# Optimization experiments

Measured on AMD Instinct MI355X. Metric: run time of the kernel, lower is better.

The kernel has to match this reference:

```python
import jax, jax.numpy as jnp
import numpy as np

B, T, DU, DM, DA, DF = 8, 2048, 512, 512, 256, 12
L_STAGES = 4   # number of routing stages
R_ITERS = 1    # diversity refinement iterations in selector
GAMMA = 1.0    # coverage_gamma
EPS = 1e-6
SCALE = float(np.sqrt(DA))


def setup_inputs() -> dict:
    key = jax.random.key(0)
    ks = jax.random.split(key, 16)
    w = lambda k, shape, fan_in: (jax.random.normal(k, shape, jnp.float32) / np.sqrt(fan_in)).astype(jnp.float32)
    return {
        'u': jax.random.normal(ks[0], (B, T, DU), jnp.float32),
        'structural_features': jax.random.normal(ks[1], (B, T, DF), jnp.float32),
        'similarity': jax.random.uniform(ks[2], (B, T, T), jnp.float32),
        'memory0': jax.random.normal(ks[3], (B, DM), jnp.float32),
        'Wq': w(ks[4], (DA, DM), DM),
        'Wk': w(ks[5], (DA, DU), DU),
        'Wv': w(ks[6], (DU, DU), DU),
        'sb_w1': w(ks[7], (DA, 3), 3),
        'sb_b1': jnp.zeros((DA,), jnp.float32),
        'sb_w2': w(ks[8], (1, DA), DA),
        'sb_b2': jnp.zeros((1,), jnp.float32),
        'log_temp': jnp.zeros((), jnp.float32),
        'W_ih': w(ks[9], (3 * DM, DU + 4), DU + 4),
        'b_ih': jnp.zeros((3 * DM,), jnp.float32),
        'W_hh': w(ks[10], (3 * DM, DM), DM),
        'b_hh': jnp.zeros((3 * DM,), jnp.float32),
    }


def _selection_stats(y, u):
    # y: [B,T], u: [B,T,DU] -> c: [B,4]
    Tn = u.shape[1]
    y_sum = jnp.maximum(y.sum(axis=1), EPS)                      # [B]
    coverage = y.sum(axis=1) / Tn
    y_norm = y / y_sum[:, None]
    entropy = -(y_norm * jnp.log(jnp.maximum(y_norm, EPS))).sum(axis=1)
    centroid = jnp.einsum('bt,btd->bd', y, u)                    # unnormalized [B,DU]
    cen = centroid / y_sum[:, None]
    dist = jnp.linalg.norm(u - cen[:, None, :], axis=-1)         # [B,T]
    spread = (y * dist).sum(axis=1) / y_sum
    wsq = (y * jnp.sum(u * u, axis=-1)).sum(axis=1)              # [B]
    csq = jnp.sum(centroid * centroid, axis=1)
    compact = 2.0 * (y_sum * wsq - csq) / jnp.maximum(y_sum * y_sum, EPS)
    return jnp.stack([coverage, entropy, spread, compact], axis=1)


def reference(u, structural_features, similarity, memory0, Wq, Wk, Wv,
              sb_w1, sb_b1, sb_w2, sb_b2, log_temp, W_ih, b_ih, W_hh, b_hh):
    k = jnp.einsum('btu,au->bta', u, Wk)                         # [B,T,DA]
    v = jnp.einsum('btu,vu->btv', u, Wv)                         # [B,T,DU]
    desc = structural_features[..., -4:-1]                       # [B,T,3]
    sbias = (jax.nn.gelu(desc @ sb_w1.T + sb_b1, approximate=False) @ sb_w2.T + sb_b2)[..., 0]
    temp = jnp.clip(jnp.exp(log_temp), 0.1, 10.0)
    memory = memory0
    prev = None
    outs = []
    for _ in range(L_STAGES):
        q = memory @ Wq.T                                        # [B,DA]
        scores = jnp.einsum('bta,ba->bt', k, q) / SCALE + sbias
        if prev is not None:
            scores = scores - GAMMA * jnp.einsum('bts,bs->bt', similarity, prev)
        logits = scores / temp
        y = jax.nn.softmax(logits, axis=1)
        for _r in range(R_ITERS):
            overlap = jnp.einsum('bts,bs->bt', similarity, y)
            penalty = overlap / jnp.maximum(jnp.max(overlap, axis=1, keepdims=True), EPS)
            logits = logits - penalty
            y = jax.nn.softmax(logits, axis=1)
        z = jnp.einsum('bt,btd->bd', y, v)                       # stage token [B,DU]
        c = _selection_stats(y, u)                               # [B,4]
        x = jnp.concatenate([z, c], axis=-1)
        gi = x @ W_ih.T + b_ih
        gh = memory @ W_hh.T + b_hh
        gir, giz, gin = jnp.split(gi, 3, axis=-1)
        ghr, ghz, ghn = jnp.split(gh, 3, axis=-1)
        rg = jax.nn.sigmoid(gir + ghr)
        zg = jax.nn.sigmoid(giz + ghz)
        ng = jnp.tanh(gin + rg * ghn)
        memory = (1.0 - zg) * ng + zg * memory                   # GRUCell update
        prev = y if prev is None else prev + y
        outs.append(z)
    return jnp.stack(outs, axis=1)                               # [B,L,DU]
```

## Files before the change

kernel.cpp:

```cpp
#include <hip/hip_runtime.h>
#include <math.h>

constexpr int cB = 8, cT = 2048, cDU = 512, cDM = 512, cDA = 256, cDF = 12, cL = 4;
constexpr float cEPS = 1e-6f;
constexpr float cSCALE = 16.0f;
constexpr float cGAMMA = 1.0f;

typedef unsigned short u16;
typedef unsigned char u8;
typedef u16 u16x8 __attribute__((ext_vector_type(8)));

constexpr size_t F_SB = 0;
constexpr size_t F_UN = F_SB + 16384;
constexpr size_t F_LG = F_UN + 16384;
constexpr size_t F_Y  = F_LG + 16384;
constexpr size_t F_PR = F_Y  + 16384;
constexpr size_t F_OV = F_PR + 16384;
constexpr size_t F_SP = F_OV + 16384;
constexpr size_t F_QK = F_SP + 256;
constexpr size_t F_M0 = F_QK + 4096;
constexpr size_t F_M1 = F_M0 + 4096;
constexpr size_t F_C  = F_M1 + 4096;
constexpr size_t F_Z  = F_C  + 4096;
constexpr size_t F_SC = F_Z  + 4096;
constexpr size_t F_A  = F_SC + 64;
constexpr size_t F_END = F_A + 262144;
constexpr size_t U_OFFB   = F_END * 4;
constexpr size_t U_BYTES  = (size_t)cB * cT * cDU * 2;
constexpr size_t S8_OFFB  = U_OFFB + U_BYTES;
constexpr size_t S8_BYTES = (size_t)cB * cT * cT;
constexpr size_t WS_NEED_U   = S8_OFFB;
constexpr size_t WS_NEED_ALL = S8_OFFB + S8_BYTES;

__device__ __forceinline__ float wave_sum(float v) {
#pragma unroll
  for (int o = 32; o; o >>= 1) v += __shfl_down(v, o);
  return v;
}
__device__ __forceinline__ u16 f2bf(float f) {
  unsigned u = __float_as_uint(f);
  return (u16)((u + 0x7fffu + ((u >> 16) & 1u)) >> 16);
}
__device__ __forceinline__ float bf2f(u16 h) { return __uint_as_float(((unsigned)h) << 16); }
__device__ __forceinline__ float dot4(float4 a, float4 b) {
  return a.x * b.x + a.y * b.y + a.z * b.z + a.w * b.w;
}
__device__ __forceinline__ unsigned pack4(float a, float b, float c, float d) {
  unsigned b0 = (unsigned)(a * 255.f + 0.5f);
  unsigned b1 = (unsigned)(b * 255.f + 0.5f);
  unsigned b2 = (unsigned)(c * 255.f + 0.5f);
  unsigned b3 = (unsigned)(d * 255.f + 0.5f);
  return b0 | (b1 << 8) | (b2 << 16) | (b3 << 24);
}
__device__ __forceinline__ void dotu8(float& sd, unsigned w, float4 p) {
  sd += (float)(w & 255u) * p.x + (float)((w >> 8) & 255u) * p.y +
        (float)((w >> 16) & 255u) * p.z + (float)(w >> 24) * p.w;
}

__global__ __launch_bounds__(256) void k_init(
    const float* __restrict__ u, const float* __restrict__ sf,
    const float* __restrict__ mem0,
    const float* __restrict__ Wq, const float* __restrict__ Wk,
    const float* __restrict__ w1, const float* __restrict__ b1,
    const float* __restrict__ w2, const float* __restrict__ b2,
    float* __restrict__ wsf, u16* __restrict__ ubf, int use_ubf) {
  const int tid = threadIdx.x;
  if (blockIdx.x >= 1024) {
    __shared__ float wkj[32][8];
    int j0 = (blockIdx.x - 1024) * 8;
    float acc[8][2] = {};
    for (int a0 = 0; a0 < cDA; a0 += 32) {
      wkj[tid >> 3][tid & 7] = Wk[(size_t)(a0 + (tid >> 3)) * cDU + j0 + (tid & 7)];
      __syncthreads();
#pragma unroll 8
      for (int aa = 0; aa < 32; ++aa) {
        float wq0 = Wq[(size_t)(a0 + aa) * cDM + tid * 2];
        float wq1 = Wq[(size_t)(a0 + aa) * cDM + tid * 2 + 1];
#pragma unroll
        for (int r = 0; r < 8; ++r) {
          acc[r][0] += wkj[aa][r] * wq0;
          acc[r][1] += wkj[aa][r] * wq1;
        }
      }
      __syncthreads();
    }
#pragma unroll
    for (int r = 0; r < 8; ++r) {
      wsf[F_A + (size_t)(j0 + r) * cDU + tid * 2] = acc[r][0];
      wsf[F_A + (size_t)(j0 + r) * cDU + tid * 2 + 1] = acc[r][1];
    }
    return;
  }
  const int gt = blockIdx.x * 256 + tid;
  const int nt = 1024 * 256;
  const int wv = tid >> 6, lane = tid & 63;
  const int gw = blockIdx.x * 4 + wv;
  const int nw = 1024 * 4;

  for (int i = gt; i < cB * cDM; i += nt) wsf[F_M0 + i] = mem0[i];

  if (use_ubf) {
    const int NU8 = cB * cT * cDU / 8;
    const float4* src = (const float4*)u;
    for (int c = gt; c < NU8; c += nt) {
      float4 f0 = src[(size_t)c * 2], f1 = src[(size_t)c * 2 + 1];
      u16x8 o;
      o[0] = f2bf(f0.x); o[1] = f2bf(f0.y); o[2] = f2bf(f0.z); o[3] = f2bf(f0.w);
      o[4] = f2bf(f1.x); o[5] = f2bf(f1.y); o[6] = f2bf(f1.z); o[7] = f2bf(f1.w);
      *(u16x8*)(ubf + (size_t)c * 8) = o;
    }
  }
  for (int row = gw; row < cB * cT; row += nw) {
    float d0 = sf[(size_t)row * cDF + 8];
    float d1 = sf[(size_t)row * cDF + 9];
    float d2 = sf[(size_t)row * cDF + 10];
    float acc = 0.f;
#pragma unroll
    for (int i = 0; i < 4; ++i) {
      int a = lane * 4 + i;
      float h = d0 * w1[a * 3 + 0] + d1 * w1[a * 3 + 1] + d2 * w1[a * 3 + 2] + b1[a];
      float g = 0.5f * h * (1.0f + erff(h * 0.70710678118654752f));
      acc += g * w2[a];
    }
    float un = 0.f;
    const float4* ur = (const float4*)(u + (size_t)row * cDU);
#pragma unroll
    for (int m = 0; m < 2; ++m) { float4 x = ur[lane + m * 64]; un += dot4(x, x); }
    acc = wave_sum(acc);
    un = wave_sum(un);
    if (lane == 0) { wsf[F_SB + row] = acc + b2[0]; wsf[F_UN + row] = un; }
  }
}

__global__ __launch_bounds__(256) void k_qk(const float* __restrict__ A,
                                            const float* __restrict__ mem,
                                            float* __restrict__ qk,
                                            float* __restrict__ c_raw) {
  int wv = threadIdx.x >> 6, lane = threadIdx.x & 63;
  int wid = blockIdx.x * 4 + wv;
  int b = wid >> 9, j = wid & 511;
  const float4* ar = (const float4*)(A + (size_t)j * cDM);
  const float4* mr = (const float4*)(mem + (size_t)b * cDM);
  float acc = dot4(ar[lane * 2], mr[lane * 2]) + dot4(ar[lane * 2 + 1], mr[lane * 2 + 1]);
  acc = wave_sum(acc);
  if (lane == 0) qk[b * cDU + j] = acc;
  int gt = blockIdx.x * 256 + threadIdx.x;
  if (gt < cB * cDU) c_raw[gt] = 0.f;
}

__global__ __launch_bounds__(256) void k_scores(
    const u16* __restrict__ ubf, const float* __restrict__ uf,
    const float* __restrict__ qk, const float* __restrict__ sbias,
    const u8* __restrict__ sim8, const float* __restrict__ simf,
    const float* __restrict__ prev, const float* __restrict__ log_temp,
    float gamma, int use_ubf, int use_s8, float* __restrict__ logits) {
  int wid = (blockIdx.x * blockDim.x + threadIdx.x) >> 6;
  int lane = threadIdx.x & 63;
  int b = wid >> 11;
  const float4* qk4 = (const float4*)(qk + (size_t)b * cDU);
  float4 q0 = qk4[lane * 2], q1 = qk4[lane * 2 + 1];
  float acc;
  if (use_ubf) {
    u16x8 s = *(const u16x8*)(ubf + (size_t)wid * cDU + lane * 8);
    acc = bf2f(s[0]) * q0.x + bf2f(s[1]) * q0.y + bf2f(s[2]) * q0.z + bf2f(s[3]) * q0.w +
          bf2f(s[4]) * q1.x + bf2f(s[5]) * q1.y + bf2f(s[6]) * q1.z + bf2f(s[7]) * q1.w;
  } else {
    const float4* ur = (const float4*)(uf + (size_t)wid * cDU);
    acc = dot4(ur[lane * 2], q0) + dot4(ur[lane * 2 + 1], q1);
  }
  acc *= (1.0f / cSCALE);
  if (gamma != 0.0f) {
    float sd = 0.f;
    const float4* pr4 = (const float4*)(prev + (size_t)b * cT);
    if (use_s8) {
#pragma unroll
      for (int m = 0; m < 2; ++m) {
        uint4 sq = *(const uint4*)(sim8 + (size_t)wid * cT + m * 1024 + lane * 16);
        const float4* pb = pr4 + m * 256 + lane * 4;
        dotu8(sd, sq.x, pb[0]); dotu8(sd, sq.y, pb[1]);
        dotu8(sd, sq.z, pb[2]); dotu8(sd, sq.w, pb[3]);
      }
      sd *= (1.0f / 255.0f);
    } else {
      const float4* sr = (const float4*)(simf + (size_t)wid * cT);
#pragma unroll
      for (int m = 0; m < 8; ++m) sd += dot4(sr[lane + m * 64], pr4[lane + m * 64]);
    }
    acc -= gamma * sd;
  }
  acc = wave_sum(acc);
  if (lane == 0) {
    float temp = fminf(fmaxf(expf(log_temp[0]), 0.1f), 10.0f);
    logits[wid] = (acc + sbias[wid]) / temp;
  }
}

__global__ __launch_bounds__(256) void k_overlap(
    const u8* __restrict__ sim8c, u8* __restrict__ sim8w,
    const float* __restrict__ simf,
    const float* __restrict__ logits, int use_s8, int convert,
    float* __restrict__ overlap) {
  __shared__ float ylds[2176];
  __shared__ float red[256];
  const int tid = threadIdx.x;
  const int wv = tid >> 6, lane = tid & 63;
  const int b = blockIdx.x >> 7;
  float l[8];
  float mx = -INFINITY;
#pragma unroll
  for (int e = 0; e < 8; ++e) { l[e] = logits[b * cT + e * 256 + tid]; mx = fmaxf(mx, l[e]); }
  red[tid] = mx; __syncthreads();
  for (int s2 = 128; s2; s2 >>= 1) { if (tid < s2) red[tid] = fmaxf(red[tid], red[tid + s2]); __syncthreads(); }
  mx = red[0]; __syncthreads();
  float sum = 0.f;
#pragma unroll
  for (int e = 0; e < 8; ++e) {
    float ev = expf(l[e] - mx);
    sum += ev;
    int s = e * 256 + tid;
    ylds[s + (s >> 4)] = ev;
  }
  red[tid] = sum; __syncthreads();
  for (int s2 = 128; s2; s2 >>= 1) { if (tid < s2) red[tid] += red[tid + s2]; __syncthreads(); }
  float invS = 1.f / red[0];
  __syncthreads();
  for (int r = 0; r < 4; ++r) {
    int row = blockIdx.x * 16 + wv * 4 + r;
    float acc = 0.f;
    if (use_s8 && !convert) {
#pragma unroll
      for (int m = 0; m < 2; ++m) {
        uint4 sq = *(const uint4*)(sim8c + (size_t)row * cT + m * 1024 + lane * 16);
        int s0 = m * 1024 + lane * 16;
#pragma unroll
        for (int k = 0; k < 4; ++k) {
          unsigned w = (&sq.x)[k];
          int s = s0 + k * 4;
          acc += (float)(w & 255u)         * ylds[s + (s >> 4)] +
                 (float)((w >> 8) & 255u)  * ylds[(s + 1) + ((s + 1) >> 4)] +
                 (float)((w >> 16) & 255u) * ylds[(s + 2) + ((s + 2) >> 4)] +
                 (float)(w >> 24)          * ylds[(s + 3) + ((s + 3) >> 4)];
        }
      }
      acc *= (1.0f / 255.0f);
    } else {
#pragma unroll
      for (int m = 0; m < 2; ++m) {
        const float4* sr = (const float4*)(simf + (size_t)row * cT + m * 1024 + lane * 16);
        uint4 oq;
#pragma unroll
        for (int k = 0; k < 4; ++k) {
          float4 sv = sr[k];
          int s = m * 1024 + lane * 16 + k * 4;
          acc += sv.x * ylds[s + (s >> 4)] + sv.y * ylds[(s + 1) + ((s + 1) >> 4)] +
                 sv.z * ylds[(s + 2) + ((s + 2) >> 4)] + sv.w * ylds[(s + 3) + ((s + 3) >> 4)];
          (&oq.x)[k] = pack4(sv.x, sv.y, sv.z, sv.w);
        }
        if (convert)
          *(uint4*)(sim8w + (size_t)row * cT + m * 1024 + lane * 16) = oq;
      }
    }
    acc = wave_sum(acc);
    if (lane == 0) overlap[row] = acc * invS;
  }
}

__global__ __launch_bounds__(256) void k_statcen(
    const float* __restrict__ overlap, const float* __restrict__ logits,
    const float* __restrict__ unorm2,
    const u16* __restrict__ ubf, const float* __restrict__ uf, int use_ubf,
    float* __restrict__ y, float* __restrict__ prev,
    float* __restrict__ scal, float* __restrict__ c_raw, int first_stage) {
  __shared__ float ylds[2048];
  __shared__ float comb[2048];
  __shared__ float red[256];
  const int tid = threadIdx.x;
  const int wv = tid >> 6, lane = tid & 63;
  const int ch = blockIdx.x, b = blockIdx.y;
  float o[8], l[8], yv[8];
  float mo = -INFINITY;
#pragma unroll
  for (int e = 0; e < 8; ++e) { o[e] = overlap[b * cT + e * 256 + tid]; mo = fmaxf(mo, o[e]); }
  red[tid] = mo; __syncthreads();
  for (int s2 = 128; s2; s2 >>= 1) { if (tid < s2) red[tid] = fmaxf(red[tid], red[tid + s2]); __syncthreads(); }
  mo = fmaxf(red[0], cEPS); __syncthreads();
  float ml = -INFINITY;
#pragma unroll
  for (int e = 0; e < 8; ++e) { l[e] = logits[b * cT + e * 256 + tid] - o[e] / mo; ml = fmaxf(ml, l[e]); }
  red[tid] = ml; __syncthreads();
  for (int s2 = 128; s2; s2 >>= 1) { if (tid < s2) red[tid] = fmaxf(red[tid], red[tid + s2]); __syncthreads(); }
  ml = red[0]; __syncthreads();
  float sum = 0.f;
#pragma unroll
  for (int e = 0; e < 8; ++e) { l[e] = expf(l[e] - ml); sum += l[e]; }
  red[tid] = sum; __syncthreads();
  for (int s2 = 128; s2; s2 >>= 1) { if (tid < s2) red[tid] += red[tid + s2]; __syncthreads(); }
  float inv = 1.f / red[0]; __syncthreads();
  float ysr_p = 0.f, wsq_p = 0.f;
#pragma unroll
  for (int e = 0; e < 8; ++e) {
    yv[e] = l[e] * inv;
    ylds[e * 256 + tid] = yv[e];
    ysr_p += yv[e];
    wsq_p += yv[e] * unorm2[b * cT + e * 256 + tid];
  }
  red[tid] = ysr_p; __syncthreads();
  for (int s2 = 128; s2; s2 >>= 1) { if (tid < s2) red[tid] += red[tid + s2]; __syncthreads(); }
  float ysr = red[0]; __syncthreads();
  float ysc = fmaxf(ysr, cEPS);
  red[tid] = wsq_p; __syncthreads();
  for (int s2 = 128; s2; s2 >>= 1) { if (tid < s2) red[tid] += red[tid + s2]; __syncthreads(); }
  float wsq = red[0]; __syncthreads();
  float ent_p = 0.f;
#pragma unroll
  for (int e = 0; e < 8; ++e) {
    float yn = yv[e] / ysc;
    ent_p -= yn * logf(fmaxf(yn, cEPS));
  }
  red[tid] = ent_p; __syncthreads();
  for (int s2 = 128; s2; s2 >>= 1) { if (tid < s2) red[tid] += red[tid + s2]; __syncthreads(); }
  float ent = red[0]; __syncthreads();
  if (ch == 0) {
#pragma unroll
    for (int e = 0; e < 8; ++e) {
      int idx = b * cT + e * 256 + tid;
      y[idx] = yv[e];
      if (first_stage) prev[idx] = yv[e]; else prev[idx] += yv[e];
    }
    if (tid == 0) {
      scal[b * 8 + 0] = ysc;
      scal[b * 8 + 1] = ysr / (float)cT;
      scal[b * 8 + 2] = ent;
      scal[b * 8 + 3] = wsq;
    }
  }
  float acc[8] = {};
  for (int i = 0; i < 16; ++i) {
    int r = ch * 64 + wv * 16 + i;
    float yvv = ylds[r];
    int row = b * cT + r;
    if (use_ubf) {
      u16x8 s8 = *(const u16x8*)(ubf + (size_t)row * cDU + lane * 8);
#pragma unroll
      for (int e = 0; e < 8; ++e) acc[e] += yvv * bf2f(s8[e]);
    } else {
      const float4* ur = (const float4*)(uf + (size_t)row * cDU);
      float4 a0 = ur[lane * 2], a1 = ur[lane * 2 + 1];
      acc[0] += yvv * a0.x; acc[1] += yvv * a0.y; acc[2] += yvv * a0.z; acc[3] += yvv * a0.w;
      acc[4] += yvv * a1.x; acc[5] += yvv * a1.y; acc[6] += yvv * a1.z; acc[7] += yvv * a1.w;
    }
  }
  __syncthreads();
#pragma unroll
  for (int e = 0; e < 8; ++e) comb[wv * 512 + lane * 8 + e] = acc[e];
  __syncthreads();
  float s0 = comb[tid] + comb[512 + tid] + comb[1024 + tid] + comb[1536 + tid];
  float s1 = comb[tid + 256] + comb[512 + tid + 256] + comb[1024 + tid + 256] + comb[1536 + tid + 256];
  atomicAdd(&c_raw[b * cDU + tid], s0);
  atomicAdd(&c_raw[b * cDU + tid + 256], s1);
}

__global__ __launch_bounds__(256) void k_zyd(
    const float* __restrict__ c_raw, const float* __restrict__ Wv,
    const u16* __restrict__ ubf, const float* __restrict__ uf, int use_ubf,
    const float* __restrict__ unorm2, const float* __restrict__ y,
    float* __restrict__ z, float* __restrict__ scal, float* __restrict__ sprp) {
  __shared__ float s4[4];
  int wv = threadIdx.x >> 6, lane = threadIdx.x & 63;
  if (blockIdx.x < 1024) {
    int wid = blockIdx.x * 4 + wv;
    int b = wid >> 9, j = wid & 511;
    const float4* c4 = (const float4*)(c_raw + (size_t)b * cDU);
    const float4* w4 = (const float4*)(Wv + (size_t)j * cDU);
    float acc = dot4(c4[lane * 2], w4[lane * 2]) + dot4(c4[lane * 2 + 1], w4[lane * 2 + 1]);
    acc = wave_sum(acc);
    if (lane == 0) z[b * cDU + j] = acc;
    return;
  }
  int unit = blockIdx.x - 1024;
  int b = unit >> 5, tc = unit & 31;
  float ysc = scal[b * 8 + 0];
  float inv = 1.f / ysc;
  const float4* c4 = (const float4*)(c_raw + (size_t)b * cDU);
  float4 cr0 = c4[lane * 2], cr1 = c4[lane * 2 + 1];
  float4 cx0, cx1;
  cx0.x = cr0.x * inv; cx0.y = cr0.y * inv; cx0.z = cr0.z * inv; cx0.w = cr0.w * inv;
  cx1.x = cr1.x * inv; cx1.y = cr1.y * inv; cx1.z = cr1.z * inv; cx1.w = cr1.w * inv;
  float cen2 = wave_sum(dot4(cx0, cx0) + dot4(cx1, cx1));
  if (tc == 0 && wv == 0) {
    float csq = wave_sum(dot4(cr0, cr0) + dot4(cr1, cr1));
    if (lane == 0) scal[b * 8 + 6] = csq;
  }
  float part = 0.f;
  for (int i = 0; i < 16; ++i) {
    int row = b * cT + tc * 64 + wv * 16 + i;
    float dot;
    if (use_ubf) {
      u16x8 s = *(const u16x8*)(ubf + (size_t)row * cDU + lane * 8);
      dot = bf2f(s[0]) * cx0.x + bf2f(s[1]) * cx0.y + bf2f(s[2]) * cx0.z + bf2f(s[3]) * cx0.w +
            bf2f(s[4]) * cx1.x + bf2f(s[5]) * cx1.y + bf2f(s[6]) * cx1.z + bf2f(s[7]) * cx1.w;
    } else {
      const float4* ur = (const float4*)(uf + (size_t)row * cDU);
      dot = dot4(ur[lane * 2], cx0) + dot4(ur[lane * 2 + 1], cx1);
    }
    dot = wave_sum(dot);
    if (lane == 0) {
      float d2 = unorm2[row] - 2.f * dot + cen2;
      part += y[row] * sqrtf(fmaxf(d2, 0.f));
    }
  }
  if (lane == 0) s4[wv] = part;
  __syncthreads();
  if (threadIdx.x == 0) sprp[b * 32 + tc] = s4[0] + s4[1] + s4[2] + s4[3];
}

__global__ __launch_bounds__(256) void k_gru(const float* __restrict__ z,
                                             const float* __restrict__ scal,
                                             const float* __restrict__ sprp,
                                             const float* __restrict__ memin,
                                             float* __restrict__ memout,
                                             const float* __restrict__ W_ih,
                                             const float* __restrict__ b_ih,
                                             const float* __restrict__ W_hh,
                                             const float* __restrict__ b_hh,
                                             float* __restrict__ out, int stage) {
  int wid = blockIdx.x * 4 + (threadIdx.x >> 6);
  int lane = threadIdx.x & 63;
  int b = wid >> 9, i = wid & 511;
  const float4* xz = (const float4*)(z + (size_t)b * cDU);
  const float4* xm = (const float4*)(memin + (size_t)b * cDM);
  float4 z0 = xz[lane * 2], z1 = xz[lane * 2 + 1];
  float4 m0 = xm[lane * 2], m1 = xm[lane * 2 + 1];
  float ysc = scal[b * 8 + 0];
  float sv = (lane < 32) ? sprp[b * 32 + lane] : 0.f;
  float spr_raw = wave_sum(sv);
  float aI[3], aH[3];
#pragma unroll
  for (int g = 0; g < 3; ++g) {
    size_t row = (size_t)(g * 512 + i);
    const float4* wI = (const float4*)(W_ih + row * 516);
    float a = dot4(z0, wI[lane * 2]) + dot4(z1, wI[lane * 2 + 1]);
    if (lane == 0) {
      float4 wt = wI[128];
      float cov = scal[b * 8 + 1], ent = scal[b * 8 + 2];
      float spr = spr_raw / ysc;
      float cmp = 2.f * (ysc * scal[b * 8 + 3] - scal[b * 8 + 6]) / fmaxf(ysc * ysc, cEPS);
      a += cov * wt.x + ent * wt.y + spr * wt.z + cmp * wt.w;
    }
    aI[g] = wave_sum(a);
    const float4* wH = (const float4*)(W_hh + row * cDM);
    float h = dot4(m0, wH[lane * 2]) + dot4(m1, wH[lane * 2 + 1]);
    aH[g] = wave_sum(h);
  }
  if (lane == 0) {
    float gir = aI[0] + b_ih[i],        ghr = aH[0] + b_hh[i];
    float giz = aI[1] + b_ih[512 + i],  ghz = aH[1] + b_hh[512 + i];
    float gin = aI[2] + b_ih[1024 + i], ghn = aH[2] + b_hh[1024 + i];
    float rg = 1.f / (1.f + expf(-(gir + ghr)));
    float zg = 1.f / (1.f + expf(-(giz + ghz)));
    float ng = tanhf(gin + rg * ghn);
    float mold = memin[b * cDM + i];
    memout[b * cDM + i] = (1.f - zg) * ng + zg * mold;
    out[(size_t)(b * cL + stage) * cDU + i] = z[b * cDU + i];
  }
}

extern "C" void kernel_launch(void* const* d_in, const int* in_sizes, int n_in,
                              void* d_out, int out_size, void* d_ws, size_t ws_size,
                              hipStream_t stream) {
  const float* u    = (const float*)d_in[0];
  const float* sf   = (const float*)d_in[1];
  const float* sim  = (const float*)d_in[2];
  const float* mem0 = (const float*)d_in[3];
  const float* Wq   = (const float*)d_in[4];
  const float* Wk   = (const float*)d_in[5];
  const float* Wv   = (const float*)d_in[6];
  const float* sbw1 = (const float*)d_in[7];
  const float* sbb1 = (const float*)d_in[8];
  const float* sbw2 = (const float*)d_in[9];
  const float* sbb2 = (const float*)d_in[10];
  const float* logt = (const float*)d_in[11];
  const float* W_ih = (const float*)d_in[12];
  const float* b_ih = (const float*)d_in[13];
  const float* W_hh = (const float*)d_in[14];
  const float* b_hh = (const float*)d_in[15];
  float* out = (float*)d_out;
  float* ws  = (float*)d_ws;
  u16* ubf  = (u16*)((char*)d_ws + U_OFFB);
  u8* sim8  = (u8*)((char*)d_ws + S8_OFFB);

  const int use_ubf = (ws_size >= WS_NEED_U) ? 1 : 0;
  const int use_s8  = (ws_size >= WS_NEED_ALL) ? 1 : 0;

  k_init<<<1088, 256, 0, stream>>>(u, sf, mem0, Wq, Wk, sbw1, sbb1, sbw2, sbb2,
                                   ws, ubf, use_ubf);

  for (int stage = 0; stage < cL; ++stage) {
    float* mcur = ws + ((stage & 1) ? F_M1 : F_M0);
    float* mnxt = ws + ((stage & 1) ? F_M0 : F_M1);
    k_qk<<<1024, 256, 0, stream>>>(ws + F_A, mcur, ws + F_QK, ws + F_C);
    k_scores<<<4096, 256, 0, stream>>>(ubf, u, ws + F_QK, ws + F_SB, sim8, sim,
                                       ws + F_PR, logt, stage == 0 ? 0.0f : cGAMMA,
                                       use_ubf, use_s8, ws + F_LG);
    k_overlap<<<1024, 256, 0, stream>>>(sim8, sim8, sim, ws + F_LG, use_s8,
                                        (stage == 0 && use_s8) ? 1 : 0, ws + F_OV);
    k_statcen<<<dim3(32, cB), 256, 0, stream>>>(ws + F_OV, ws + F_LG, ws + F_UN,
                                                ubf, u, use_ubf,
                                                ws + F_Y, ws + F_PR, ws + F_SC, ws + F_C,
                                                stage == 0 ? 1 : 0);
    k_zyd<<<1280, 256, 0, stream>>>(ws + F_C, Wv, ubf, u, use_ubf,
                                    ws + F_UN, ws + F_Y, ws + F_Z, ws + F_SC, ws + F_SP);
    k_gru<<<1024, 256, 0, stream>>>(ws + F_Z, ws + F_SC, ws + F_SP, mcur, mnxt,
                                    W_ih, b_ih, W_hh, b_hh, out, stage);
  }
}
```

Measured before the change: 503.4 us.

## Fuse per-stage kernels into one persistent cooperative kernel with grid syncs

Replaces the six per-stage kernel launches (qk, scores, overlap, statcen, zyd, gru) across four stages with one cooperative persistent kernel that loops over stages and phases and separates them with grid-wide barriers. The aim is to remove about 24 launch overheads and the pipeline drains between dependent small kernels. Work is redistributed over a grid sized from occupancy, capped at 1024 blocks, and the spread partials are now per-row-group (4096 entries) rather than 256. In exchange, each grid sync costs something, parallelism is capped by co-residency, and the cached static block count assumes occupancy never changes.

```diff
diff --git a/kernel.cpp b/kernel.cpp
--- a/kernel.cpp
+++ b/kernel.cpp
@@ -1,5 +1,8 @@
 #include <hip/hip_runtime.h>
+#include <hip/hip_cooperative_groups.h>
 #include <math.h>
+
+namespace cg = cooperative_groups;
 
 constexpr int cB = 8, cT = 2048, cDU = 512, cDM = 512, cDA = 256, cDF = 12, cL = 4;
 constexpr float cEPS = 1e-6f;
@@ -17,7 +20,7 @@
 constexpr size_t F_PR = F_Y  + 16384;
 constexpr size_t F_OV = F_PR + 16384;
 constexpr size_t F_SP = F_OV + 16384;
-constexpr size_t F_QK = F_SP + 256;
+constexpr size_t F_QK = F_SP + 4096;
 constexpr size_t F_M0 = F_QK + 4096;
 constexpr size_t F_M1 = F_M0 + 4096;
 constexpr size_t F_C  = F_M1 + 4096;
@@ -36,6 +39,25 @@
 #pragma unroll
   for (int o = 32; o; o >>= 1) v += __shfl_down(v, o);
   return v;
+}
+__device__ __forceinline__ float wave_max(float v) {
+#pragma unroll
+  for (int o = 32; o; o >>= 1) v = fmaxf(v, __shfl_down(v, o));
+  return v;
+}
+__device__ __forceinline__ float blk_max(float v, float* red, int wv, int lane) {
+  v = wave_max(v);
+  __syncthreads();
+  if (lane == 0) red[wv] = v;
+  __syncthreads();
+  return fmaxf(fmaxf(red[0], red[1]), fmaxf(red[2], red[3]));
+}
+__device__ __forceinline__ float blk_sum(float v, float* red, int wv, int lane) {
+  v = wave_sum(v);
+  __syncthreads();
+  if (lane == 0) red[wv] = v;
+  __syncthreads();
+  return red[0] + red[1] + red[2] + red[3];
 }
 __device__ __forceinline__ u16 f2bf(float f) {
   unsigned u = __float_as_uint(f);
@@ -95,7 +117,7 @@
   const int nt = 1024 * 256;
   const int wv = tid >> 6, lane = tid & 63;
   const int gw = blockIdx.x * 4 + wv;
-  const int nw = 1024 * 4;
+  const int nwv = 1024 * 4;
 
   for (int i = gt; i < cB * cDM; i += nt) wsf[F_M0 + i] = mem0[i];
 
@@ -110,7 +132,7 @@
       *(u16x8*)(ubf + (size_t)c * 8) = o;
     }
   }
-  for (int row = gw; row < cB * cT; row += nw) {
+  for (int row = gw; row < cB * cT; row += nwv) {
     float d0 = sf[(size_t)row * cDF + 8];
     float d1 = sf[(size_t)row * cDF + 9];
     float d2 = sf[(size_t)row * cDF + 10];
@@ -132,336 +154,324 @@
   }
 }
 
-__global__ __launch_bounds__(256) void k_qk(const float* __restrict__ A,
-                                            const float* __restrict__ mem,
-                                            float* __restrict__ qk,
-                                            float* __restrict__ c_raw) {
-  int wv = threadIdx.x >> 6, lane = threadIdx.x & 63;
-  int wid = blockIdx.x * 4 + wv;
-  int b = wid >> 9, j = wid & 511;
-  const float4* ar = (const float4*)(A + (size_t)j * cDM);
-  const float4* mr = (const float4*)(mem + (size_t)b * cDM);
-  float acc = dot4(ar[lane * 2], mr[lane * 2]) + dot4(ar[lane * 2 + 1], mr[lane * 2 + 1]);
-  acc = wave_sum(acc);
-  if (lane == 0) qk[b * cDU + j] = acc;
-  int gt = blockIdx.x * 256 + threadIdx.x;
-  if (gt < cB * cDU) c_raw[gt] = 0.f;
-}
-
-__global__ __launch_bounds__(256) void k_scores(
-    const u16* __restrict__ ubf, const float* __restrict__ uf,
-    const float* __restrict__ qk, const float* __restrict__ sbias,
-    const u8* __restrict__ sim8, const float* __restrict__ simf,
-    const float* __restrict__ prev, const float* __restrict__ log_temp,
-    float gamma, int use_ubf, int use_s8, float* __restrict__ logits) {
-  int wid = (blockIdx.x * blockDim.x + threadIdx.x) >> 6;
-  int lane = threadIdx.x & 63;
-  int b = wid >> 11;
-  const float4* qk4 = (const float4*)(qk + (size_t)b * cDU);
-  float4 q0 = qk4[lane * 2], q1 = qk4[lane * 2 + 1];
-  float acc;
-  if (use_ubf) {
-    u16x8 s = *(const u16x8*)(ubf + (size_t)wid * cDU + lane * 8);
-    acc = bf2f(s[0]) * q0.x + bf2f(s[1]) * q0.y + bf2f(s[2]) * q0.z + bf2f(s[3]) * q0.w +
-          bf2f(s[4]) * q1.x + bf2f(s[5]) * q1.y + bf2f(s[6]) * q1.z + bf2f(s[7]) * q1.w;
-  } else {
-    const float4* ur = (const float4*)(uf + (size_t)wid * cDU);
-    acc = dot4(ur[lane * 2], q0) + dot4(ur[lane * 2 + 1], q1);
-  }
-  acc *= (1.0f / cSCALE);
-  if (gamma != 0.0f) {
-    float sd = 0.f;
-    const float4* pr4 = (const float4*)(prev + (size_t)b * cT);
-    if (use_s8) {
-#pragma unroll
-      for (int m = 0; m < 2; ++m) {
-        uint4 sq = *(const uint4*)(sim8 + (size_t)wid * cT + m * 1024 + lane * 16);
-        const float4* pb = pr4 + m * 256 + lane * 4;
-        dotu8(sd, sq.x, pb[0]); dotu8(sd, sq.y, pb[1]);
-        dotu8(sd, sq.z, pb[2]); dotu8(sd, sq.w, pb[3]);
-      }
-      sd *= (1.0f / 255.0f);
-    } else {
-      const float4* sr = (const float4*)(simf + (size_t)wid * cT);
-#pragma unroll
-      for (int m = 0; m < 8; ++m) sd += dot4(sr[lane + m * 64], pr4[lane + m * 64]);
-    }
-    acc -= gamma * sd;
-  }
-  acc = wave_sum(acc);
-  if (lane == 0) {
-    float temp = fminf(fmaxf(expf(log_temp[0]), 0.1f), 10.0f);
-    logits[wid] = (acc + sbias[wid]) / temp;
-  }
-}
-
-__global__ __launch_bounds__(256) void k_overlap(
-    const u8* __restrict__ sim8c, u8* __restrict__ sim8w,
-    const float* __restrict__ simf,
-    const float* __restrict__ logits, int use_s8, int convert,
-    float* __restrict__ overlap) {
-  __shared__ float ylds[2176];
-  __shared__ float red[256];
+__global__ __launch_bounds__(256, 4) void k_main(
+    const float* __restrict__ u, const float* __restrict__ sim,
+    const float* __restrict__ logt, const float* __restrict__ Wv,
+    const float* __restrict__ W_ih, const float* __restrict__ b_ih,
+    const float* __restrict__ W_hh, const float* __restrict__ b_hh,
+    float* __restrict__ ws, u16* __restrict__ ubf, u8* __restrict__ sim8,
+    float* __restrict__ out, int use_ubf, int use_s8) {
+  cg::grid_group gg = cg::this_grid();
+  __shared__ float lds[4104];
+  float* red = lds + 4096;
   const int tid = threadIdx.x;
   const int wv = tid >> 6, lane = tid & 63;
-  const int b = blockIdx.x >> 7;
-  float l[8];
-  float mx = -INFINITY;
-#pragma unroll
-  for (int e = 0; e < 8; ++e) { l[e] = logits[b * cT + e * 256 + tid]; mx = fmaxf(mx, l[e]); }
-  red[tid] = mx; __syncthreads();
-  for (int s2 = 128; s2; s2 >>= 1) { if (tid < s2) red[tid] = fmaxf(red[tid], red[tid + s2]); __syncthreads(); }
-  mx = red[0]; __syncthreads();
-  float sum = 0.f;
-#pragma unroll
-  for (int e = 0; e < 8; ++e) {
-    float ev = expf(l[e] - mx);
-    sum += ev;
-    int s = e * 256 + tid;
-    ylds[s + (s >> 4)] = ev;
-  }
-  red[tid] = sum; __syncthreads();
-  for (int s2 = 128; s2; s2 >>= 1) { if (tid < s2) red[tid] += red[tid + s2]; __syncthreads(); }
-  float invS = 1.f / red[0];
-  __syncthreads();
-  for (int r = 0; r < 4; ++r) {
-    int row = blockIdx.x * 16 + wv * 4 + r;
-    float acc = 0.f;
-    if (use_s8 && !convert) {
-#pragma unroll
-      for (int m = 0; m < 2; ++m) {
-        uint4 sq = *(const uint4*)(sim8c + (size_t)row * cT + m * 1024 + lane * 16);
-        int s0 = m * 1024 + lane * 16;
-#pragma unroll
-        for (int k = 0; k < 4; ++k) {
-          unsigned w = (&sq.x)[k];
-          int s = s0 + k * 4;
-          acc += (float)(w & 255u)         * ylds[s + (s >> 4)] +
-                 (float)((w >> 8) & 255u)  * ylds[(s + 1) + ((s + 1) >> 4)] +
-                 (float)((w >> 16) & 255u) * ylds[(s + 2) + ((s + 2) >> 4)] +
-                 (float)(w >> 24)          * ylds[(s + 3) + ((s + 3) >> 4)];
-        }
-      }
-      acc *= (1.0f / 255.0f);
-    } else {
-#pragma unroll
-      for (int m = 0; m < 2; ++m) {
-        const float4* sr = (const float4*)(simf + (size_t)row * cT + m * 1024 + lane * 16);
-        uint4 oq;
-#pragma unroll
-        for (int k = 0; k < 4; ++k) {
-          float4 sv = sr[k];
-          int s = m * 1024 + lane * 16 + k * 4;
-          acc += sv.x * ylds[s + (s >> 4)] + sv.y * ylds[(s + 1) + ((s + 1) >> 4)] +
-                 sv.z * ylds[(s + 2) + ((s + 2) >> 4)] + sv.w * ylds[(s + 3) + ((s + 3) >> 4)];
-          (&oq.x)[k] = pack4(sv.x, sv.y, sv.z, sv.w);
-        }
-        if (convert)
-          *(uint4*)(sim8w + (size_t)row * cT + m * 1024 + lane * 16) = oq;
-      }
-    }
-    acc = wave_sum(acc);
-    if (lane == 0) overlap[row] = acc * invS;
-  }
-}
-
-__global__ __launch_bounds__(256) void k_statcen(
-    const float* __restrict__ overlap, const float* __restrict__ logits,
-    const float* __restrict__ unorm2,
-    const u16* __restrict__ ubf, const float* __restrict__ uf, int use_ubf,
-    float* __restrict__ y, float* __restrict__ prev,
-    float* __restrict__ scal, float* __restrict__ c_raw, int first_stage) {
-  __shared__ float ylds[2048];
-  __shared__ float comb[2048];
-  __shared__ float red[256];
-  const int tid = threadIdx.x;
-  const int wv = tid >> 6, lane = tid & 63;
-  const int ch = blockIdx.x, b = blockIdx.y;
-  float o[8], l[8], yv[8];
-  float mo = -INFINITY;
-#pragma unroll
-  for (int e = 0; e < 8; ++e) { o[e] = overlap[b * cT + e * 256 + tid]; mo = fmaxf(mo, o[e]); }
-  red[tid] = mo; __syncthreads();
-  for (int s2 = 128; s2; s2 >>= 1) { if (tid < s2) red[tid] = fmaxf(red[tid], red[tid + s2]); __syncthreads(); }
-  mo = fmaxf(red[0], cEPS); __syncthreads();
-  float ml = -INFINITY;
-#pragma unroll
-  for (int e = 0; e < 8; ++e) { l[e] = logits[b * cT + e * 256 + tid] - o[e] / mo; ml = fmaxf(ml, l[e]); }
-  red[tid] = ml; __syncthreads();
-  for (int s2 = 128; s2; s2 >>= 1) { if (tid < s2) red[tid] = fmaxf(red[tid], red[tid + s2]); __syncthreads(); }
-  ml = red[0]; __syncthreads();
-  float sum = 0.f;
-#pragma unroll
-  for (int e = 0; e < 8; ++e) { l[e] = expf(l[e] - ml); sum += l[e]; }
-  red[tid] = sum; __syncthreads();
-  for (int s2 = 128; s2; s2 >>= 1) { if (tid < s2) red[tid] += red[tid + s2]; __syncthreads(); }
-  float inv = 1.f / red[0]; __syncthreads();
-  float ysr_p = 0.f, wsq_p = 0.f;
-#pragma unroll
-  for (int e = 0; e < 8; ++e) {
-    yv[e] = l[e] * inv;
-    ylds[e * 256 + tid] = yv[e];
-    ysr_p += yv[e];
-    wsq_p += yv[e] * unorm2[b * cT + e * 256 + tid];
-  }
-  red[tid] = ysr_p; __syncthreads();
-  for (int s2 = 128; s2; s2 >>= 1) { if (tid < s2) red[tid] += red[tid + s2]; __syncthreads(); }
-  float ysr = red[0]; __syncthreads();
-  float ysc = fmaxf(ysr, cEPS);
-  red[tid] = wsq_p; __syncthreads();
-  for (int s2 = 128; s2; s2 >>= 1) { if (tid < s2) red[tid] += red[tid + s2]; __syncthreads(); }
-  float wsq = red[0]; __syncthreads();
-  float ent_p = 0.f;
-#pragma unroll
-  for (int e = 0; e < 8; ++e) {
-    float yn = yv[e] / ysc;
-    ent_p -= yn * logf(fmaxf(yn, cEPS));
-  }
-  red[tid] = ent_p; __syncthreads();
-  for (int s2 = 128; s2; s2 >>= 1) { if (tid < s2) red[tid] += red[tid + s2]; __syncthreads(); }
-  float ent = red[0]; __syncthreads();
-  if (ch == 0) {
-#pragma unroll
-    for (int e = 0; e < 8; ++e) {
-      int idx = b * cT + e * 256 + tid;
-      y[idx] = yv[e];
-      if (first_stage) prev[idx] = yv[e]; else prev[idx] += yv[e];
-    }
-    if (tid == 0) {
-      scal[b * 8 + 0] = ysc;
-      scal[b * 8 + 1] = ysr / (float)cT;
-      scal[b * 8 + 2] = ent;
-      scal[b * 8 + 3] = wsq;
-    }
-  }
-  float acc[8] = {};
-  for (int i = 0; i < 16; ++i) {
-    int r = ch * 64 + wv * 16 + i;
-    float yvv = ylds[r];
-    int row = b * cT + r;
-    if (use_ubf) {
-      u16x8 s8 = *(const u16x8*)(ubf + (size_t)row * cDU + lane * 8);
-#pragma unroll
-      for (int e = 0; e < 8; ++e) acc[e] += yvv * bf2f(s8[e]);
-    } else {
-      const float4* ur = (const float4*)(uf + (size_t)row * cDU);
-      float4 a0 = ur[lane * 2], a1 = ur[lane * 2 + 1];
-      acc[0] += yvv * a0.x; acc[1] += yvv * a0.y; acc[2] += yvv * a0.z; acc[3] += yvv * a0.w;
-      acc[4] += yvv * a1.x; acc[5] += yvv * a1.y; acc[6] += yvv * a1.z; acc[7] += yvv * a1.w;
-    }
-  }
-  __syncthreads();
-#pragma unroll
-  for (int e = 0; e < 8; ++e) comb[wv * 512 + lane * 8 + e] = acc[e];
-  __syncthreads();
-  float s0 = comb[tid] + comb[512 + tid] + comb[1024 + tid] + comb[1536 + tid];
-  float s1 = comb[tid + 256] + comb[512 + tid + 256] + comb[1024 + tid + 256] + comb[1536 + tid + 256];
-  atomicAdd(&c_raw[b * cDU + tid], s0);
-  atomicAdd(&c_raw[b * cDU + tid + 256], s1);
-}
-
-__global__ __launch_bounds__(256) void k_zyd(
-    const float* __restrict__ c_raw, const float* __restrict__ Wv,
-    const u16* __restrict__ ubf, const float* __restrict__ uf, int use_ubf,
-    const float* __restrict__ unorm2, const float* __restrict__ y,
-    float* __restrict__ z, float* __restrict__ scal, float* __restrict__ sprp) {
-  __shared__ float s4[4];
-  int wv = threadIdx.x >> 6, lane = threadIdx.x & 63;
-  if (blockIdx.x < 1024) {
-    int wid = blockIdx.x * 4 + wv;
-    int b = wid >> 9, j = wid & 511;
-    const float4* c4 = (const float4*)(c_raw + (size_t)b * cDU);
-    const float4* w4 = (const float4*)(Wv + (size_t)j * cDU);
-    float acc = dot4(c4[lane * 2], w4[lane * 2]) + dot4(c4[lane * 2 + 1], w4[lane * 2 + 1]);
-    acc = wave_sum(acc);
-    if (lane == 0) z[b * cDU + j] = acc;
-    return;
-  }
-  int unit = blockIdx.x - 1024;
-  int b = unit >> 5, tc = unit & 31;
-  float ysc = scal[b * 8 + 0];
-  float inv = 1.f / ysc;
-  const float4* c4 = (const float4*)(c_raw + (size_t)b * cDU);
-  float4 cr0 = c4[lane * 2], cr1 = c4[lane * 2 + 1];
-  float4 cx0, cx1;
-  cx0.x = cr0.x * inv; cx0.y = cr0.y * inv; cx0.z = cr0.z * inv; cx0.w = cr0.w * inv;
-  cx1.x = cr1.x * inv; cx1.y = cr1.y * inv; cx1.z = cr1.z * inv; cx1.w = cr1.w * inv;
-  float cen2 = wave_sum(dot4(cx0, cx0) + dot4(cx1, cx1));
-  if (tc == 0 && wv == 0) {
-    float csq = wave_sum(dot4(cr0, cr0) + dot4(cr1, cr1));
-    if (lane == 0) scal[b * 8 + 6] = csq;
-  }
-  float part = 0.f;
-  for (int i = 0; i < 16; ++i) {
-    int row = b * cT + tc * 64 + wv * 16 + i;
-    float dot;
-    if (use_ubf) {
-      u16x8 s = *(const u16x8*)(ubf + (size_t)row * cDU + lane * 8);
-      dot = bf2f(s[0]) * cx0.x + bf2f(s[1]) * cx0.y + bf2f(s[2]) * cx0.z + bf2f(s[3]) * cx0.w +
-            bf2f(s[4]) * cx1.x + bf2f(s[5]) * cx1.y + bf2f(s[6]) * cx1.z + bf2f(s[7]) * cx1.w;
-    } else {
-      const float4* ur = (const float4*)(uf + (size_t)row * cDU);
-      dot = dot4(ur[lane * 2], cx0) + dot4(ur[lane * 2 + 1], cx1);
-    }
-    dot = wave_sum(dot);
-    if (lane == 0) {
-      float d2 = unorm2[row] - 2.f * dot + cen2;
-      part += y[row] * sqrtf(fmaxf(d2, 0.f));
-    }
-  }
-  if (lane == 0) s4[wv] = part;
-  __syncthreads();
-  if (threadIdx.x == 0) sprp[b * 32 + tc] = s4[0] + s4[1] + s4[2] + s4[3];
-}
-
-__global__ __launch_bounds__(256) void k_gru(const float* __restrict__ z,
-                                             const float* __restrict__ scal,
-                                             const float* __restrict__ sprp,
-                                             const float* __restrict__ memin,
-                                             float* __restrict__ memout,
-                                             const float* __restrict__ W_ih,
-                                             const float* __restrict__ b_ih,
-                                             const float* __restrict__ W_hh,
-                                             const float* __restrict__ b_hh,
-                                             float* __restrict__ out, int stage) {
-  int wid = blockIdx.x * 4 + (threadIdx.x >> 6);
-  int lane = threadIdx.x & 63;
-  int b = wid >> 9, i = wid & 511;
-  const float4* xz = (const float4*)(z + (size_t)b * cDU);
-  const float4* xm = (const float4*)(memin + (size_t)b * cDM);
-  float4 z0 = xz[lane * 2], z1 = xz[lane * 2 + 1];
-  float4 m0 = xm[lane * 2], m1 = xm[lane * 2 + 1];
-  float ysc = scal[b * 8 + 0];
-  float sv = (lane < 32) ? sprp[b * 32 + lane] : 0.f;
-  float spr_raw = wave_sum(sv);
-  float aI[3], aH[3];
-#pragma unroll
-  for (int g = 0; g < 3; ++g) {
-    size_t row = (size_t)(g * 512 + i);
-    const float4* wI = (const float4*)(W_ih + row * 516);
-    float a = dot4(z0, wI[lane * 2]) + dot4(z1, wI[lane * 2 + 1]);
-    if (lane == 0) {
-      float4 wt = wI[128];
-      float cov = scal[b * 8 + 1], ent = scal[b * 8 + 2];
-      float spr = spr_raw / ysc;
-      float cmp = 2.f * (ysc * scal[b * 8 + 3] - scal[b * 8 + 6]) / fmaxf(ysc * ysc, cEPS);
-      a += cov * wt.x + ent * wt.y + spr * wt.z + cmp * wt.w;
-    }
-    aI[g] = wave_sum(a);
-    const float4* wH = (const float4*)(W_hh + row * cDM);
-    float h = dot4(m0, wH[lane * 2]) + dot4(m1, wH[lane * 2 + 1]);
-    aH[g] = wave_sum(h);
-  }
-  if (lane == 0) {
-    float gir = aI[0] + b_ih[i],        ghr = aH[0] + b_hh[i];
-    float giz = aI[1] + b_ih[512 + i],  ghz = aH[1] + b_hh[512 + i];
-    float gin = aI[2] + b_ih[1024 + i], ghn = aH[2] + b_hh[1024 + i];
-    float rg = 1.f / (1.f + expf(-(gir + ghr)));
-    float zg = 1.f / (1.f + expf(-(giz + ghz)));
-    float ng = tanhf(gin + rg * ghn);
-    float mold = memin[b * cDM + i];
-    memout[b * cDM + i] = (1.f - zg) * ng + zg * mold;
-    out[(size_t)(b * cL + stage) * cDU + i] = z[b * cDU + i];
+  const int wid = blockIdx.x * 4 + wv;
+  const int nw = gridDim.x * 4;
+
+  const float temp = fminf(fmaxf(expf(logt[0]), 0.1f), 10.0f);
+
+  for (int stage = 0; stage < cL; ++stage) {
+    float* mcur = ws + ((stage & 1) ? F_M1 : F_M0);
+    float* mnxt = ws + ((stage & 1) ? F_M0 : F_M1);
+    const int convert = (stage == 0 && use_s8) ? 1 : 0;
+
+    {
+      for (int t = wid; t < cB * cDM; t += nw) {
+        int b = t >> 9, j = t & 511;
+        const float4* ar = (const float4*)(ws + F_A + (size_t)j * cDM);
+        const float4* mr = (const float4*)(mcur + (size_t)b * cDM);
+        float acc = dot4(ar[lane * 2], mr[lane * 2]) + dot4(ar[lane * 2 + 1], mr[lane * 2 + 1]);
+        acc = wave_sum(acc);
+        if (lane == 0) ws[F_QK + t] = acc;
+      }
+      for (int t = blockIdx.x * 256 + tid; t < cB * cDU; t += gridDim.x * 256)
+        ws[F_C + t] = 0.f;
+    }
+    gg.sync();
+
+    {
+      for (int s = wid; s < 4096; s += nw) {
+        const int b = s >> 9;
+        const float4* qk4 = (const float4*)(ws + F_QK + (size_t)b * cDU);
+        float4 q0 = qk4[lane * 2], q1 = qk4[lane * 2 + 1];
+        float4 pv[8];
+        if (stage > 0 && use_s8) {
+          const float4* pr4 = (const float4*)(ws + F_PR + (size_t)b * cT);
+#pragma unroll
+          for (int m = 0; m < 2; ++m)
+#pragma unroll
+            for (int k = 0; k < 4; ++k) pv[m * 4 + k] = pr4[m * 256 + lane * 4 + k];
+        }
+#pragma unroll
+        for (int i = 0; i < 4; ++i) {
+          int grow = s * 4 + i;
+          float acc;
+          if (use_ubf) {
+            u16x8 sv = *(const u16x8*)(ubf + (size_t)grow * cDU + lane * 8);
+            acc = bf2f(sv[0]) * q0.x + bf2f(sv[1]) * q0.y + bf2f(sv[2]) * q0.z + bf2f(sv[3]) * q0.w +
+                  bf2f(sv[4]) * q1.x + bf2f(sv[5]) * q1.y + bf2f(sv[6]) * q1.z + bf2f(sv[7]) * q1.w;
+          } else {
+            const float4* ur = (const float4*)(u + (size_t)grow * cDU);
+            acc = dot4(ur[lane * 2], q0) + dot4(ur[lane * 2 + 1], q1);
+          }
+          acc *= (1.0f / cSCALE);
+          if (stage > 0) {
+            float sd = 0.f;
+            if (use_s8) {
+              const u8* sr = sim8 + (size_t)grow * cT;
+              uint4 sq0 = *(const uint4*)(sr + lane * 16);
+              uint4 sq1 = *(const uint4*)(sr + 1024 + lane * 16);
+              dotu8(sd, sq0.x, pv[0]); dotu8(sd, sq0.y, pv[1]);
+              dotu8(sd, sq0.z, pv[2]); dotu8(sd, sq0.w, pv[3]);
+              dotu8(sd, sq1.x, pv[4]); dotu8(sd, sq1.y, pv[5]);
+              dotu8(sd, sq1.z, pv[6]); dotu8(sd, sq1.w, pv[7]);
+              sd *= (1.0f / 255.0f);
+            } else {
+              const float4* sr = (const float4*)(sim + (size_t)grow * cT);
+              const float4* pr4 = (const float4*)(ws + F_PR + (size_t)b * cT);
+#pragma unroll
+              for (int m = 0; m < 8; ++m) sd += dot4(sr[lane + m * 64], pr4[lane + m * 64]);
+            }
+            acc -= cGAMMA * sd;
+          }
+          acc = wave_sum(acc);
+          if (lane == 0) ws[F_LG + grow] = (acc + ws[F_SB + grow]) / temp;
+        }
+      }
+    }
+    gg.sync();
+
+    {
+      for (int bx = blockIdx.x; bx < 1024; bx += gridDim.x) {
+        const int b = bx >> 7;
+        float l[8];
+        float mx = -INFINITY;
+#pragma unroll
+        for (int e = 0; e < 8; ++e) { l[e] = ws[F_LG + b * cT + e * 256 + tid]; mx = fmaxf(mx, l[e]); }
+        mx = blk_max(mx, red, wv, lane);
+        float sum = 0.f;
+#pragma unroll
+        for (int e = 0; e < 8; ++e) {
+          float ev = expf(l[e] - mx);
+          sum += ev;
+          int sidx = e * 256 + tid;
+          lds[sidx + (sidx >> 4)] = ev;
+        }
+        sum = blk_sum(sum, red, wv, lane);
+        float invS = 1.f / sum;
+        for (int r = 0; r < 4; ++r) {
+          int row = bx * 16 + wv * 4 + r;
+          float acc = 0.f;
+          if (use_s8 && !convert) {
+            const u8* sr = sim8 + (size_t)row * cT;
+#pragma unroll
+            for (int m = 0; m < 2; ++m) {
+              uint4 sq = *(const uint4*)(sr + m * 1024 + lane * 16);
+              int s0 = m * 1024 + lane * 16;
+#pragma unroll
+              for (int k = 0; k < 4; ++k) {
+                unsigned w = (&sq.x)[k];
+                int si = s0 + k * 4;
+                acc += (float)(w & 255u)         * lds[si + (si >> 4)] +
+                       (float)((w >> 8) & 255u)  * lds[(si + 1) + ((si + 1) >> 4)] +
+                       (float)((w >> 16) & 255u) * lds[(si + 2) + ((si + 2) >> 4)] +
+                       (float)(w >> 24)          * lds[(si + 3) + ((si + 3) >> 4)];
+              }
+            }
+            acc *= (1.0f / 255.0f);
+          } else {
+            const float4* sr = (const float4*)(sim + (size_t)row * cT);
+#pragma unroll
+            for (int m = 0; m < 2; ++m) {
+              uint4 oq;
+#pragma unroll
+              for (int k = 0; k < 4; ++k) {
+                float4 sv = sr[m * 256 + lane * 4 + k];
+                int si = m * 1024 + lane * 16 + k * 4;
+                acc += sv.x * lds[si + (si >> 4)] + sv.y * lds[(si + 1) + ((si + 1) >> 4)] +
+                       sv.z * lds[(si + 2) + ((si + 2) >> 4)] + sv.w * lds[(si + 3) + ((si + 3) >> 4)];
+                (&oq.x)[k] = pack4(sv.x, sv.y, sv.z, sv.w);
+              }
+              if (convert)
+                *(uint4*)(sim8 + (size_t)row * cT + m * 1024 + lane * 16) = oq;
+            }
+          }
+          acc = wave_sum(acc);
+          if (lane == 0) ws[F_OV + row] = acc * invS;
+        }
+      }
+    }
+    gg.sync();
+
+    {
+      for (int bx = blockIdx.x; bx < 1024; bx += gridDim.x) {
+        const int b = bx >> 7, ch = bx & 127;
+        float o[8], l[8], yv8[8];
+        float mo = -INFINITY;
+#pragma unroll
+        for (int e = 0; e < 8; ++e) { o[e] = ws[F_OV + b * cT + e * 256 + tid]; mo = fmaxf(mo, o[e]); }
+        mo = fmaxf(blk_max(mo, red, wv, lane), cEPS);
+        float ml = -INFINITY;
+#pragma unroll
+        for (int e = 0; e < 8; ++e) { l[e] = ws[F_LG + b * cT + e * 256 + tid] - o[e] / mo; ml = fmaxf(ml, l[e]); }
+        ml = blk_max(ml, red, wv, lane);
+        float sum = 0.f;
+#pragma unroll
+        for (int e = 0; e < 8; ++e) { l[e] = expf(l[e] - ml); sum += l[e]; }
+        sum = blk_sum(sum, red, wv, lane);
+        float inv = 1.f / sum;
+        float ysr_p = 0.f, wsq_p = 0.f;
+#pragma unroll
+        for (int e = 0; e < 8; ++e) {
+          yv8[e] = l[e] * inv;
+          lds[e * 256 + tid] = yv8[e];
+          ysr_p += yv8[e];
+          wsq_p += yv8[e] * ws[F_UN + b * cT + e * 256 + tid];
+        }
+        float ysr = blk_sum(ysr_p, red, wv, lane);
+        float ysc = fmaxf(ysr, cEPS);
+        float wsq = blk_sum(wsq_p, red, wv, lane);
+        float ent_p = 0.f;
+#pragma unroll
+        for (int e = 0; e < 8; ++e) {
+          float yn = yv8[e] / ysc;
+          ent_p -= yn * logf(fmaxf(yn, cEPS));
+        }
+        float ent = blk_sum(ent_p, red, wv, lane);
+        if (ch == 0) {
+#pragma unroll
+          for (int e = 0; e < 8; ++e) {
+            int idx = b * cT + e * 256 + tid;
+            ws[F_Y + idx] = yv8[e];
+            if (stage == 0) ws[F_PR + idx] = yv8[e]; else ws[F_PR + idx] += yv8[e];
+          }
+          if (tid == 0) {
+            ws[F_SC + b * 8 + 0] = ysc;
+            ws[F_SC + b * 8 + 1] = ysr / (float)cT;
+            ws[F_SC + b * 8 + 2] = ent;
+            ws[F_SC + b * 8 + 3] = wsq;
+          }
+        }
+        float acc[8] = {};
+        for (int i = 0; i < 4; ++i) {
+          int r = ch * 16 + wv * 4 + i;
+          float yvv = lds[r];
+          int row = b * cT + r;
+          if (use_ubf) {
+            u16x8 s8v = *(const u16x8*)(ubf + (size_t)row * cDU + lane * 8);
+#pragma unroll
+            for (int e = 0; e < 8; ++e) acc[e] += yvv * bf2f(s8v[e]);
+          } else {
+            const float4* ur = (const float4*)(u + (size_t)row * cDU);
+            float4 a0 = ur[lane * 2], a1 = ur[lane * 2 + 1];
+            acc[0] += yvv * a0.x; acc[1] += yvv * a0.y; acc[2] += yvv * a0.z; acc[3] += yvv * a0.w;
+            acc[4] += yvv * a1.x; acc[5] += yvv * a1.y; acc[6] += yvv * a1.z; acc[7] += yvv * a1.w;
+          }
+        }
+        __syncthreads();
+#pragma unroll
+        for (int e = 0; e < 8; ++e) lds[2048 + wv * 512 + lane * 8 + e] = acc[e];
+        __syncthreads();
+        float s0 = lds[2048 + tid] + lds[2048 + 512 + tid] + lds[2048 + 1024 + tid] + lds[2048 + 1536 + tid];
+        float s1 = lds[2048 + tid + 256] + lds[2048 + 512 + tid + 256] +
+                   lds[2048 + 1024 + tid + 256] + lds[2048 + 1536 + tid + 256];
+        atomicAdd(&ws[F_C + b * cDU + tid], s0);
+        atomicAdd(&ws[F_C + b * cDU + tid + 256], s1);
+      }
+    }
+    gg.sync();
+
+    {
+      for (int t = wid; t < cB * cDU; t += nw) {
+        int b = t >> 9, j = t & 511;
+        const float4* c4 = (const float4*)(ws + F_C + (size_t)b * cDU);
+        const float4* w4 = (const float4*)(Wv + (size_t)j * cDU);
+        float acc = dot4(c4[lane * 2], w4[lane * 2]) + dot4(c4[lane * 2 + 1], w4[lane * 2 + 1]);
+        acc = wave_sum(acc);
+        if (lane == 0) ws[F_Z + t] = acc;
+      }
+      for (int s = wid; s < 4096; s += nw) {
+        int b = s >> 9, loc = s & 511;
+        float ysc = ws[F_SC + b * 8 + 0];
+        float inv = 1.f / ysc;
+        const float4* c4 = (const float4*)(ws + F_C + (size_t)b * cDU);
+        float4 cr0 = c4[lane * 2], cr1 = c4[lane * 2 + 1];
+        float4 cx0, cx1;
+        cx0.x = cr0.x * inv; cx0.y = cr0.y * inv; cx0.z = cr0.z * inv; cx0.w = cr0.w * inv;
+        cx1.x = cr1.x * inv; cx1.y = cr1.y * inv; cx1.z = cr1.z * inv; cx1.w = cr1.w * inv;
+        float cen2 = wave_sum(dot4(cx0, cx0) + dot4(cx1, cx1));
+        if (loc == 0) {
+          float csq = wave_sum(dot4(cr0, cr0) + dot4(cr1, cr1));
+          if (lane == 0) ws[F_SC + b * 8 + 6] = csq;
+        }
+        float part = 0.f;
+        for (int i = 0; i < 4; ++i) {
+          int row = b * cT + loc * 4 + i;
+          float dot;
+          if (use_ubf) {
+            u16x8 sv = *(const u16x8*)(ubf + (size_t)row * cDU + lane * 8);
+            dot = bf2f(sv[0]) * cx0.x + bf2f(sv[1]) * cx0.y + bf2f(sv[2]) * cx0.z + bf2f(sv[3]) * cx0.w +
+                  bf2f(sv[4]) * cx1.x + bf2f(sv[5]) * cx1.y + bf2f(sv[6]) * cx1.z + bf2f(sv[7]) * cx1.w;
+          } else {
+            const float4* ur = (const float4*)(u + (size_t)row * cDU);
+            dot = dot4(ur[lane * 2], cx0) + dot4(ur[lane * 2 + 1], cx1);
+          }
+          dot = wave_sum(dot);
+          if (lane == 0) {
+            float d2 = ws[F_UN + row] - 2.f * dot + cen2;
+            part += ws[F_Y + row] * sqrtf(fmaxf(d2, 0.f));
+          }
+        }
+        if (lane == 0) ws[F_SP + s] = part;
+      }
+    }
+    gg.sync();
+
+    {
+      for (int t = wid; t < cB * cDM; t += nw) {
+        int b = t >> 9, i = t & 511;
+        const float4* xz = (const float4*)(ws + F_Z + (size_t)b * cDU);
+        const float4* xm = (const float4*)(mcur + (size_t)b * cDM);
+        float4 z0 = xz[lane * 2], z1 = xz[lane * 2 + 1];
+        float4 m0 = xm[lane * 2], m1 = xm[lane * 2 + 1];
+        float ysc = ws[F_SC + b * 8 + 0];
+        float sv_ = 0.f;
+#pragma unroll
+        for (int k2 = 0; k2 < 8; ++k2) sv_ += ws[F_SP + b * 512 + lane * 8 + k2];
+        float spr_raw = wave_sum(sv_);
+        float aI[3], aH[3];
+#pragma unroll
+        for (int g = 0; g < 3; ++g) {
+          size_t rrow = (size_t)(g * 512 + i);
+          const float4* wI = (const float4*)(W_ih + rrow * 516);
+          float a = dot4(z0, wI[lane * 2]) + dot4(z1, wI[lane * 2 + 1]);
+          if (lane == 0) {
+            float4 wt = wI[128];
+            float cov = ws[F_SC + b * 8 + 1], ent = ws[F_SC + b * 8 + 2];
+            float spr = spr_raw / ysc;
+            float cmp = 2.f * (ysc * ws[F_SC + b * 8 + 3] - ws[F_SC + b * 8 + 6]) / fmaxf(ysc * ysc, cEPS);
+            a += cov * wt.x + ent * wt.y + spr * wt.z + cmp * wt.w;
+          }
+          aI[g] = wave_sum(a);
+          const float4* wH = (const float4*)(W_hh + rrow * cDM);
+          float h = dot4(m0, wH[lane * 2]) + dot4(m1, wH[lane * 2 + 1]);
+          aH[g] = wave_sum(h);
+        }
+        if (lane == 0) {
+          float gir = aI[0] + b_ih[i],        ghr = aH[0] + b_hh[i];
+          float giz = aI[1] + b_ih[512 + i],  ghz = aH[1] + b_hh[512 + i];
+          float gin = aI[2] + b_ih[1024 + i], ghn = aH[2] + b_hh[1024 + i];
+          float rg = 1.f / (1.f + expf(-(gir + ghr)));
+          float zg = 1.f / (1.f + expf(-(giz + ghz)));
+          float ng = tanhf(gin + rg * ghn);
+          float mold = mcur[b * cDM + i];
+          mnxt[b * cDM + i] = (1.f - zg) * ng + zg * mold;
+          out[(size_t)(b * cL + stage) * cDU + i] = ws[F_Z + b * cDU + i];
+        }
+      }
+    }
+    if (stage < cL - 1) gg.sync();
   }
 }
 
@@ -489,28 +499,24 @@
   u16* ubf  = (u16*)((char*)d_ws + U_OFFB);
   u8* sim8  = (u8*)((char*)d_ws + S8_OFFB);
 
-  const int use_ubf = (ws_size >= WS_NEED_U) ? 1 : 0;
-  const int use_s8  = (ws_size >= WS_NEED_ALL) ? 1 : 0;
+  int use_ubf = (ws_size >= WS_NEED_U) ? 1 : 0;
+  int use_s8  = (ws_size >= WS_NEED_ALL) ? 1 : 0;
 
   k_init<<<1088, 256, 0, stream>>>(u, sf, mem0, Wq, Wk, sbw1, sbb1, sbw2, sbb2,
                                    ws, ubf, use_ubf);
 
-  for (int stage = 0; stage < cL; ++stage) {
-    float* mcur = ws + ((stage & 1) ? F_M1 : F_M0);
-    float* mnxt = ws + ((stage & 1) ? F_M0 : F_M1);
-    k_qk<<<1024, 256, 0, stream>>>(ws + F_A, mcur, ws + F_QK, ws + F_C);
-    k_scores<<<4096, 256, 0, stream>>>(ubf, u, ws + F_QK, ws + F_SB, sim8, sim,
-                                       ws + F_PR, logt, stage == 0 ? 0.0f : cGAMMA,
-                                       use_ubf, use_s8, ws + F_LG);
-    k_overlap<<<1024, 256, 0, stream>>>(sim8, sim8, sim, ws + F_LG, use_s8,
-                                        (stage == 0 && use_s8) ? 1 : 0, ws + F_OV);
-    k_statcen<<<dim3(32, cB), 256, 0, stream>>>(ws + F_OV, ws + F_LG, ws + F_UN,
-                                                ubf, u, use_ubf,
-                                                ws + F_Y, ws + F_PR, ws + F_SC, ws + F_C,
-                                                stage == 0 ? 1 : 0);
-    k_zyd<<<1280, 256, 0, stream>>>(ws + F_C, Wv, ubf, u, use_ubf,
-                                    ws + F_UN, ws + F_Y, ws + F_Z, ws + F_SC, ws + F_SP);
-    k_gru<<<1024, 256, 0, stream>>>(ws + F_Z, ws + F_SC, ws + F_SP, mcur, mnxt,
-                                    W_ih, b_ih, W_hh, b_hh, out, stage);
+  static int nblk = 0;
+  if (nblk == 0) {
+    int occ = 0;
+    if (hipOccupancyMaxActiveBlocksPerMultiprocessor(&occ, (const void*)k_main, 256, 0) != hipSuccess || occ <= 0)
+      occ = 1;
+    nblk = occ * 256;
+    if (nblk > 1024) nblk = 1024;
+    if (nblk < 256) nblk = 256;
   }
-}
+  void* kargs[] = {(void*)&u, (void*)&sim, (void*)&logt, (void*)&Wv,
+                   (void*)&W_ih, (void*)&b_ih, (void*)&W_hh, (void*)&b_hh,
+                   (void*)&ws, (void*)&ubf, (void*)&sim8, (void*)&out,
+                   (void*)&use_ubf, (void*)&use_s8};
+  hipLaunchCooperativeKernel((const void*)k_main, dim3(nblk), dim3(256), kargs, 0, stream);
+}
```

Result: slower. 1.775 ms (+252.7%).
